# Performance work log

Hardware: AMD Instinct MI355X
Metric: run time of the kernel (lower is better)

Reference implementation:

```python
import jax, jax.numpy as jnp
import numpy as np

N_NODES = 100000
N_EDGES = 1600000
N_GRAPHS = 2048
F_IN = 33
D = 256


def _graph_conv(x, edge_index, w_rel, b_rel, w_root):
    # PyG GraphConv (aggr='add'): out = lin_rel(sum_j x_j) + lin_root(x)
    src, dst = edge_index[0], edge_index[1]
    agg = jax.ops.segment_sum(x[src], dst, num_segments=x.shape[0])  # [N, F]
    return agg @ w_rel + b_rel + x @ w_root


def setup_inputs() -> dict:
    key = jax.random.key(0)
    ks = jax.random.split(key, 16)
    scale_in = 1.0 / np.sqrt(F_IN)
    scale_d = 1.0 / np.sqrt(D)
    inp = {
        "x": jax.random.normal(ks[0], (N_NODES, F_IN), dtype=jnp.float32),
        "edge_index": jax.random.randint(ks[1], (2, N_EDGES), 0, N_NODES),
        "batch_index": jnp.sort(jax.random.randint(ks[2], (N_NODES,), 0, N_GRAPHS)),
        # initial_conv: GraphConv(F_IN -> D)
        "w_rel0": jax.random.normal(ks[3], (F_IN, D), dtype=jnp.float32) * scale_in,
        "b_rel0": jnp.zeros((D,), dtype=jnp.float32),
        "w_root0": jax.random.normal(ks[4], (F_IN, D), dtype=jnp.float32) * scale_in,
        # conv1..conv3: GraphConv(D -> D)
        "w_rel1": jax.random.normal(ks[5], (D, D), dtype=jnp.float32) * scale_d,
        "b_rel1": jnp.zeros((D,), dtype=jnp.float32),
        "w_root1": jax.random.normal(ks[6], (D, D), dtype=jnp.float32) * scale_d,
        "w_rel2": jax.random.normal(ks[7], (D, D), dtype=jnp.float32) * scale_d,
        "b_rel2": jnp.zeros((D,), dtype=jnp.float32),
        "w_root2": jax.random.normal(ks[8], (D, D), dtype=jnp.float32) * scale_d,
        "w_rel3": jax.random.normal(ks[9], (D, D), dtype=jnp.float32) * scale_d,
        "b_rel3": jnp.zeros((D,), dtype=jnp.float32),
        "w_root3": jax.random.normal(ks[10], (D, D), dtype=jnp.float32) * scale_d,
        # output head Linear(D -> 1)
        "w_out": jax.random.normal(ks[11], (D, 1), dtype=jnp.float32) * scale_d,
        "b_out": jnp.zeros((1,), dtype=jnp.float32),
    }
    return inp


def reference(x, edge_index, batch_index,
              w_rel0, b_rel0, w_root0,
              w_rel1, b_rel1, w_root1,
              w_rel2, b_rel2, w_root2,
              w_rel3, b_rel3, w_root3,
              w_out, b_out):
    # dropout omitted (eval mode)
    h = jax.nn.gelu(_graph_conv(x, edge_index, w_rel0, b_rel0, w_root0))
    h = jax.nn.gelu(_graph_conv(h, edge_index, w_rel1, b_rel1, w_root1))
    h = jax.nn.gelu(_graph_conv(h, edge_index, w_rel2, b_rel2, w_root2))
    h = jax.nn.gelu(_graph_conv(h, edge_index, w_rel3, b_rel3, w_root3))
    # global mean pool over graphs
    sums = jax.ops.segment_sum(h, batch_index, num_segments=N_GRAPHS)          # [G, D]
    counts = jax.ops.segment_sum(jnp.ones((h.shape[0],), h.dtype), batch_index,
                                 num_segments=N_GRAPHS)                         # [G]
    pooled = sums / jnp.maximum(counts, 1.0)[:, None]
    return pooled @ w_out + b_out                                               # [G, 1]
```

## Files before the change

kernel.cpp:

```cpp
#include <hip/hip_runtime.h>
#include <math.h>

#define NN 100000
#define NE 1600000
#define NG 2048
#define FIN 33
#define DD 256

#define SH 8
#define NB ((NN + 255) >> 8)
#define CH 4096
#define PCAP 4608
#define ESCAP 6144

#define RBLKS ((NN + 255) / 256)

typedef __attribute__((ext_vector_type(8))) short bf16x8;
typedef __attribute__((ext_vector_type(4))) float f32x4;

__device__ __forceinline__ float b2f(unsigned short u){
    union { unsigned int i; float f; } c; c.i = ((unsigned int)u) << 16; return c.f;
}
__device__ __forceinline__ unsigned short f2b(float f){
    union { float f; unsigned int u; } c; c.f = f;
    unsigned int r = c.u + 0x7fffu + ((c.u >> 16) & 1u);
    return (unsigned short)(r >> 16);
}

__device__ __forceinline__ float gelu_tanh(float x){
    float x3 = x * x * x;
    float t = tanhf(0.7978845608028654f * (x + 0.044715f * x3));
    return 0.5f * x * (1.0f + t);
}

__global__ __launch_bounds__(256) void k_bin(const int* __restrict__ src,
                                             const int* __restrict__ dst,
                                             int* __restrict__ gcur,
                                             int* __restrict__ pairs){
    __shared__ int cnt[NB];
    __shared__ int lb[NB];
    __shared__ int gbase[NB];
    __shared__ int sc[512];
    __shared__ int2 stage[CH];

    int t = threadIdx.x;
    for(int i = t; i < NB; i += 256) cnt[i] = 0;
    __syncthreads();

    int e0 = blockIdx.x * CH;
    int n = NE - e0; if(n > CH) n = CH;

    int  myb[16];
    int  myr[16];
    int2 myp[16];
    #pragma unroll
    for(int k = 0; k < 16; k++){
        int e = e0 + t + k * 256;
        if(e < NE){
            int s = src[e], d = dst[e];
            int b = d >> SH;
            myr[k] = atomicAdd(&cnt[b], 1);
            myb[k] = b;
            myp[k] = make_int2(s, d);
        } else myb[k] = -1;
    }
    __syncthreads();

    sc[t]       = (t       < NB) ? cnt[t]       : 0;
    sc[t + 256] = (t + 256 < NB) ? cnt[t + 256] : 0;
    __syncthreads();
    for(int off = 1; off < 512; off <<= 1){
        int a  = (t >= off)       ? sc[t - off]       : 0;
        int b2 = (t + 256 >= off) ? sc[t + 256 - off] : 0;
        __syncthreads();
        sc[t] += a; sc[t + 256] += b2;
        __syncthreads();
    }
    for(int i = t; i < NB; i += 256){
        lb[i] = sc[i] - cnt[i];
        int c = cnt[i];
        gbase[i] = (c > 0) ? atomicAdd(&gcur[i], c) : 0;
    }
    __syncthreads();

    #pragma unroll
    for(int k = 0; k < 16; k++){
        if(myb[k] >= 0) stage[lb[myb[k]] + myr[k]] = myp[k];
    }
    __syncthreads();

    for(int i = t; i < n; i += 256){
        int2 p = stage[i];
        int b = p.y >> SH;
        int tgt = gbase[b] + (i - lb[b]);
        if(tgt < PCAP) pairs[(size_t)b * PCAP + tgt] = p.x | ((p.y & 255) << 17);
    }
}

__global__ void k_sscan(const int* __restrict__ gcur, int* __restrict__ boff){
    __shared__ int s[512];
    int t = threadIdx.x;
    int v = 0;
    if(t < NB){ v = gcur[t]; if(v > PCAP) v = PCAP; }
    s[t] = v; __syncthreads();
    for(int off = 1; off < 512; off <<= 1){
        int u = (t >= off) ? s[t - off] : 0;
        __syncthreads();
        s[t] += u;
        __syncthreads();
    }
    if(t < NB) boff[t] = s[t] - v;
}

__global__ __launch_bounds__(256) void k_bcsr(const int* __restrict__ pairs,
                                              const int* __restrict__ gcur,
                                              const int* __restrict__ boff,
                                              int* __restrict__ deg,
                                              int* __restrict__ rs,
                                              int* __restrict__ esrc){
    __shared__ int hist[256];
    __shared__ int sc[256];
    __shared__ int cur2[256];
    __shared__ int est[ESCAP];

    int b = blockIdx.x;
    int t = threadIdx.x;
    int m = gcur[b]; if(m > PCAP) m = PCAP;
    int pstart = boff[b];
    const int* bp = pairs + (size_t)b * PCAP;

    hist[t] = 0;
    __syncthreads();
    for(int i = t; i < m; i += 256) atomicAdd(&hist[(bp[i] >> 17) & 255], 1);
    __syncthreads();

    sc[t] = hist[t]; __syncthreads();
    for(int off = 1; off < 256; off <<= 1){
        int u = (t >= off) ? sc[t - off] : 0;
        __syncthreads();
        sc[t] += u;
        __syncthreads();
    }
    int excl = sc[t] - hist[t];
    cur2[t] = excl;
    int node = (b << 8) + t;
    if(node < NN){
        deg[node] = hist[t];
        rs[node]  = pstart + excl;
    }
    __syncthreads();

    for(int i = t; i < m; i += 256){
        int p = bp[i];
        int pos = atomicAdd(&cur2[(p >> 17) & 255], 1);
        int s = p & 0x1FFFF;
        if(pos < ESCAP) est[pos] = s;
        else esrc[pstart + pos] = s;
    }
    __syncthreads();
    int lim = (m < ESCAP) ? m : ESCAP;
    for(int i = t; i < lim; i += 256) esrc[pstart + i] = est[i];
}

__global__ void k_xpad(const float* __restrict__ x, unsigned short* __restrict__ xb){
    int idx = blockIdx.x * 256 + threadIdx.x;
    if(idx >= NN * 64) return;
    int n = idx >> 6, c = idx & 63;
    xb[idx] = (c < FIN) ? f2b(x[(size_t)n * FIN + c]) : 0;
}

__global__ void k_aggx(const unsigned short* __restrict__ xb, const int* __restrict__ rs,
                       const int* __restrict__ deg, const int* __restrict__ esrc,
                       unsigned short* __restrict__ axb){
    int wv = (blockIdx.x * blockDim.x + threadIdx.x) >> 6;
    int lane = threadIdx.x & 63;
    int node = wv * 4 + (lane >> 4);
    int l16 = lane & 15;
    if(node >= NN) return;
    int start = rs[node], cnt = deg[node];
    float a0 = 0.f, a1 = 0.f, a2 = 0.f, a3 = 0.f;
    const unsigned short* xp = xb + l16 * 4;
    int j = 0;
    for(; j + 4 <= cnt; j += 4){
        int e0 = esrc[start+j], e1 = esrc[start+j+1], e2 = esrc[start+j+2], e3 = esrc[start+j+3];
        ushort4 v0 = *(const ushort4*)(xp + (size_t)e0 * 64);
        ushort4 v1 = *(const ushort4*)(xp + (size_t)e1 * 64);
        ushort4 v2 = *(const ushort4*)(xp + (size_t)e2 * 64);
        ushort4 v3 = *(const ushort4*)(xp + (size_t)e3 * 64);
        a0 += (b2f(v0.x) + b2f(v1.x)) + (b2f(v2.x) + b2f(v3.x));
        a1 += (b2f(v0.y) + b2f(v1.y)) + (b2f(v2.y) + b2f(v3.y));
        a2 += (b2f(v0.z) + b2f(v1.z)) + (b2f(v2.z) + b2f(v3.z));
        a3 += (b2f(v0.w) + b2f(v1.w)) + (b2f(v2.w) + b2f(v3.w));
    }
    for(; j < cnt; j++){
        int e = esrc[start + j];
        ushort4 v = *(const ushort4*)(xp + (size_t)e * 64);
        a0 += b2f(v.x); a1 += b2f(v.y); a2 += b2f(v.z); a3 += b2f(v.w);
    }
    ushort4 o; o.x = f2b(a0); o.y = f2b(a1); o.z = f2b(a2); o.w = f2b(a3);
    *(ushort4*)(axb + (size_t)node * 64 + l16 * 4) = o;
}

__global__ void k_agg256(const unsigned short* __restrict__ h, const int* __restrict__ rs,
                         const int* __restrict__ deg, const int* __restrict__ esrc,
                         unsigned short* __restrict__ agg){
    int wv = (blockIdx.x * blockDim.x + threadIdx.x) >> 6;
    int lane = threadIdx.x & 63;
    int node = wv * 2 + (lane >> 5);
    int l32 = lane & 31;
    if(node >= NN) return;
    int start = rs[node], cnt = deg[node];
    float a[8] = {0.f,0.f,0.f,0.f,0.f,0.f,0.f,0.f};
    const unsigned short* hp = h + l32 * 8;
    int j = 0;
    for(; j + 8 <= cnt; j += 8){
        bf16x8 v[8];
        #pragma unroll
        for(int q = 0; q < 8; q++){
            int e = esrc[start + j + q];
            v[q] = *(const bf16x8*)(hp + (size_t)e * DD);
        }
        #pragma unroll
        for(int q = 0; q < 8; q++)
            #pragma unroll
            for(int d = 0; d < 8; d++)
                a[d] += b2f((unsigned short)v[q][d]);
    }
    for(; j < cnt; j++){
        int e = esrc[start + j];
        bf16x8 v = *(const bf16x8*)(hp + (size_t)e * DD);
        #pragma unroll
        for(int d = 0; d < 8; d++) a[d] += b2f((unsigned short)v[d]);
    }
    bf16x8 o;
    #pragma unroll
    for(int d = 0; d < 8; d++) o[d] = (short)f2b(a[d]);
    *(bf16x8*)(agg + (size_t)node * DD + l32 * 8) = o;
}

struct WPtrs { const float* w[6]; };

__global__ void k_wt6(WPtrs wp, unsigned short* __restrict__ btAll){
    __shared__ float s[16][17];
    const float* W = wp.w[blockIdx.z];
    unsigned short* Bt = btAll + (size_t)blockIdx.z * DD * DD;
    int tx = threadIdx.x, ty = threadIdx.y;
    int k = blockIdx.y * 16 + ty;
    int j = blockIdx.x * 16 + tx;
    s[ty][tx] = W[k * DD + j];
    __syncthreads();
    Bt[(size_t)(blockIdx.x * 16 + ty) * DD + blockIdx.y * 16 + tx] = f2b(s[tx][ty]);
}

struct W2Ptrs { const float* w[2]; };

__global__ void k_wt0(W2Ptrs wp, unsigned short* __restrict__ btAll){
    int idx = blockIdx.x * 256 + threadIdx.x;
    if(idx >= DD * 64) return;
    const float* W = wp.w[blockIdx.z];
    unsigned short* Bt = btAll + (size_t)blockIdx.z * DD * 64;
    int j = idx >> 6, k = idx & 63;
    Bt[idx] = (k < FIN) ? f2b(W[(size_t)k * DD + j]) : 0;
}

__global__ void k_cnt(const int* __restrict__ batch, int* __restrict__ gcnt){
    int i = blockIdx.x * 256 + threadIdx.x;
    if(i < NN) atomicAdd(&gcnt[batch[i]], 1);
}

template<int KS, int AST, bool POOL>
__global__ __launch_bounds__(512, 4) void k_mfma_gemm(
    const unsigned short* __restrict__ A0, const unsigned short* __restrict__ A1,
    const unsigned short* __restrict__ Bt0, const unsigned short* __restrict__ Bt1,
    const float* __restrict__ bias, unsigned short* __restrict__ out,
    const int* __restrict__ batch, const float* __restrict__ wout,
    float* __restrict__ gsum)
{
    constexpr int CK  = KS * 32;
    constexpr int BST = CK + 8;
    constexpr int SEG = CK / 8;
    __shared__ unsigned short Bs[128 * BST];

    int t = threadIdx.x;
    int lane = t & 63;
    int w = t >> 6;
    int r16 = lane & 15;
    int kg  = lane >> 4;

    int bid = blockIdx.x;
    int rblk = (bid >> 4) * 8 + (bid & 7);
    int chalf = (bid >> 3) & 1;
    if(rblk >= RBLKS) return;
    int i0 = rblk * 256;
    int jbase = chalf * 128;
    int baseRow = i0 + w * 32;

    f32x4 acc[2][8];
    #pragma unroll
    for(int m = 0; m < 2; m++)
        #pragma unroll
        for(int n = 0; n < 8; n++)
            acc[m][n] = (f32x4){0.f, 0.f, 0.f, 0.f};

    auto loadA = [&](int gks, bf16x8* af){
        const unsigned short* Ap = (gks < KS) ? A0 : A1;
        int kk = ((gks < KS) ? gks : gks - KS) * 32 + kg * 8;
        #pragma unroll
        for(int m = 0; m < 2; m++){
            int gi = baseRow + m * 16 + r16;
            if(gi > NN - 1) gi = NN - 1;
            af[m] = *(const bf16x8*)(Ap + (size_t)gi * AST + kk);
        }
    };

    bf16x8 afb[2][2];
    loadA(0, afb[0]);
    loadA(1, afb[1]);

    #pragma unroll
    for(int c = 0; c < 2; c++){
        const unsigned short* Bp = c ? Bt1 : Bt0;
        if(c) __syncthreads();
        #pragma unroll
        for(int p = 0; p < (128 * SEG) / 512; p++){
            int idx = p * 512 + t;
            int row = idx / SEG;
            int k8 = (idx % SEG) * 8;
            *(bf16x8*)(&Bs[row * BST + k8]) =
                *(const bf16x8*)(Bp + (size_t)(jbase + row) * AST + k8);
        }
        __syncthreads();
        #pragma unroll
        for(int ksl = 0; ksl < KS; ksl++){
            int gks = c * KS + ksl;
            __builtin_amdgcn_s_setprio(1);
            #pragma unroll
            for(int n = 0; n < 8; n++){
                bf16x8 bfr = *(const bf16x8*)(&Bs[(n * 16 + r16) * BST + ksl * 32 + kg * 8]);
                acc[0][n] = __builtin_amdgcn_mfma_f32_16x16x32_bf16(afb[gks & 1][0], bfr, acc[0][n], 0, 0, 0);
                acc[1][n] = __builtin_amdgcn_mfma_f32_16x16x32_bf16(afb[gks & 1][1], bfr, acc[1][n], 0, 0, 0);
            }
            __builtin_amdgcn_s_setprio(0);
            if(gks + 2 < 2 * KS) loadA(gks + 2, afb[gks & 1]);
        }
    }

    int rg = kg * 4;
    if constexpr (!POOL){
        #pragma unroll
        for(int n = 0; n < 8; n++){
            int gj = jbase + n * 16 + r16;
            float bb = bias[gj];
            #pragma unroll
            for(int m = 0; m < 2; m++){
                #pragma unroll
                for(int r = 0; r < 4; r++){
                    int gi = baseRow + m * 16 + rg + r;
                    if(gi < NN)
                        out[(size_t)gi * DD + gj] = f2b(gelu_tanh(acc[m][n][r] + bb));
                }
            }
        }
    } else {
        #pragma unroll
        for(int m = 0; m < 2; m++){
            #pragma unroll
            for(int r = 0; r < 4; r++){
                float s = 0.f;
                #pragma unroll
                for(int n = 0; n < 8; n++){
                    int gj = jbase + n * 16 + r16;
                    s += gelu_tanh(acc[m][n][r] + bias[gj]) * wout[gj];
                }
                s += __shfl_xor(s, 1);
                s += __shfl_xor(s, 2);
                s += __shfl_xor(s, 4);
                s += __shfl_xor(s, 8);
                int gi = baseRow + m * 16 + rg + r;
                if(r16 == 0 && gi < NN)
                    atomicAdd(&gsum[batch[gi]], s);
            }
        }
    }
}

__global__ void k_final(const float* __restrict__ gsum, const int* __restrict__ gcnt,
                        const float* __restrict__ bout, float* __restrict__ out){
    int g = blockIdx.x * 256 + threadIdx.x;
    if(g < NG) out[g] = gsum[g] / fmaxf((float)gcnt[g], 1.f) + bout[0];
}

extern "C" void kernel_launch(void* const* d_in, const int* in_sizes, int n_in,
                              void* d_out, int out_size, void* d_ws, size_t ws_size,
                              hipStream_t stream){
    const float* x       = (const float*)d_in[0];
    const int*   ei      = (const int*)d_in[1];
    const int*   src     = ei;
    const int*   dst     = ei + NE;
    const int*   batch   = (const int*)d_in[2];
    const float* w_rel0  = (const float*)d_in[3];
    const float* b_rel0  = (const float*)d_in[4];
    const float* w_root0 = (const float*)d_in[5];
    const float* w_rel1  = (const float*)d_in[6];
    const float* b_rel1  = (const float*)d_in[7];
    const float* w_root1 = (const float*)d_in[8];
    const float* w_rel2  = (const float*)d_in[9];
    const float* b_rel2  = (const float*)d_in[10];
    const float* w_root2 = (const float*)d_in[11];
    const float* w_rel3  = (const float*)d_in[12];
    const float* b_rel3  = (const float*)d_in[13];
    const float* w_root3 = (const float*)d_in[14];
    const float* w_out   = (const float*)d_in[15];
    const float* b_out   = (const float*)d_in[16];
    float* out = (float*)d_out;

    char* ws = (char*)d_ws;
    size_t off = 0;
    auto alloc = [&](size_t bytes) -> void* {
        void* p = ws + off;
        off = (off + bytes + 255) & ~(size_t)255;
        return p;
    };
    unsigned short* hA  = (unsigned short*)alloc((size_t)NN * DD * 2);
    unsigned short* hB  = (unsigned short*)alloc((size_t)NN * DD * 2);
    unsigned short* agg = (unsigned short*)alloc((size_t)NN * DD * 2);
    int*   deg  = (int*)alloc((size_t)NN * 4);
    int*   rs   = (int*)alloc((size_t)NN * 4);
    int*   esrc = (int*)alloc((size_t)NE * 4);
    int*   gcur = (int*)alloc(512 * 4);
    int*   boff = (int*)alloc(512 * 4);
    float* gsum = (float*)alloc((size_t)NG * 4);
    int*   gcnt = (int*)alloc((size_t)NG * 4);
    unsigned short* btAll = (unsigned short*)alloc((size_t)6 * DD * DD * 2);
    unsigned short* bt0All = (unsigned short*)alloc((size_t)2 * DD * 64 * 2);
    (void)ws_size; (void)in_sizes; (void)n_in; (void)out_size;

    int* pairs = (int*)hB;
    unsigned short* xb  = agg;
    unsigned short* axb = agg + (size_t)NN * 64 + 128;

    hipMemsetAsync(gcur, 0, 512 * 4, stream);
    k_bin<<<(NE + CH - 1) / CH, 256, 0, stream>>>(src, dst, gcur, pairs);
    k_sscan<<<1, 512, 0, stream>>>(gcur, boff);
    k_bcsr<<<NB, 256, 0, stream>>>(pairs, gcur, boff, deg, rs, esrc);

    size_t poolBytes = (size_t)((char*)(gcnt + NG) - (char*)gsum);
    hipMemsetAsync(gsum, 0, poolBytes, stream);
    k_cnt<<<(NN + 255) / 256, 256, 0, stream>>>(batch, gcnt);

    WPtrs wp; wp.w[0] = w_rel1; wp.w[1] = w_root1; wp.w[2] = w_rel2;
    wp.w[3] = w_root2; wp.w[4] = w_rel3; wp.w[5] = w_root3;
    k_wt6<<<dim3(16, 16, 6), dim3(16, 16), 0, stream>>>(wp, btAll);
    W2Ptrs w2; w2.w[0] = w_rel0; w2.w[1] = w_root0;
    k_wt0<<<dim3((DD * 64 + 255) / 256, 1, 2), 256, 0, stream>>>(w2, bt0All);
    k_xpad<<<(NN * 64 + 255) / 256, 256, 0, stream>>>(x, xb);

    unsigned short* bt[6];
    for(int i = 0; i < 6; i++) bt[i] = btAll + (size_t)i * DD * DD;
    unsigned short* bt0r = bt0All;
    unsigned short* bt0o = bt0All + (size_t)DD * 64;

    int agg2Grid = (NN * 32 + 255) / 256;
    int gemmGrid = ((RBLKS + 7) / 8) * 16;

    k_aggx<<<(NN + 15) / 16, 256, 0, stream>>>(xb, rs, deg, esrc, axb);
    k_mfma_gemm<2, 64, false><<<gemmGrid, 512, 0, stream>>>(axb, xb, bt0r, bt0o, b_rel0, hA,
                                                            batch, w_out, gsum);
    k_agg256<<<agg2Grid, 256, 0, stream>>>(hA, rs, deg, esrc, agg);
    k_mfma_gemm<8, 256, false><<<gemmGrid, 512, 0, stream>>>(agg, hA, bt[0], bt[1], b_rel1, hB,
                                                             batch, w_out, gsum);
    k_agg256<<<agg2Grid, 256, 0, stream>>>(hB, rs, deg, esrc, agg);
    k_mfma_gemm<8, 256, false><<<gemmGrid, 512, 0, stream>>>(agg, hB, bt[2], bt[3], b_rel2, hA,
                                                             batch, w_out, gsum);
    k_agg256<<<agg2Grid, 256, 0, stream>>>(hA, rs, deg, esrc, agg);
    k_mfma_gemm<8, 256, true><<<gemmGrid, 512, 0, stream>>>(agg, hA, bt[4], bt[5], b_rel3, hB,
                                                            batch, w_out, gsum);

    k_final<<<(NG + 255) / 256, 256, 0, stream>>>(gsum, gcnt, b_out, out);
}
```

Measured before the change: 776.6 us.

## Fuse neighbor aggregation into GEMM via LDS-staged aggregated tile

Replaces the separate aggregation kernel and GEMM for the 256-wide layers with a fused kernel. Each 128-row block gathers neighbor sums into a swizzled LDS tile, then runs MFMA with B fragments read straight from global memory instead of staged in LDS. This avoids the global round-trip of the aggregated matrix and three kernel launches, at the cost of a 64KB LDS footprint that limits occupancy and B reads that go uncached through LDS. GELU is also rewritten in a sigmoid/exp form, which is algebraically equivalent to the tanh form.

```diff
diff --git a/kernel.cpp b/kernel.cpp
--- a/kernel.cpp
+++ b/kernel.cpp
@@ -14,6 +14,7 @@
 #define ESCAP 6144
 
 #define RBLKS ((NN + 255) / 256)
+#define FBLKS ((NN + 127) / 128)
 
 typedef __attribute__((ext_vector_type(8))) short bf16x8;
 typedef __attribute__((ext_vector_type(4))) float f32x4;
@@ -28,9 +29,8 @@
 }
 
 __device__ __forceinline__ float gelu_tanh(float x){
-    float x3 = x * x * x;
-    float t = tanhf(0.7978845608028654f * (x + 0.044715f * x3));
-    return 0.5f * x * (1.0f + t);
+    float z = 0.7978845608028654f * (x + 0.044715f * x * x * x);
+    return x / (1.0f + __expf(-2.0f * z));
 }
 
 __global__ __launch_bounds__(256) void k_bin(const int* __restrict__ src,
@@ -201,43 +201,6 @@
     *(ushort4*)(axb + (size_t)node * 64 + l16 * 4) = o;
 }
 
-__global__ void k_agg256(const unsigned short* __restrict__ h, const int* __restrict__ rs,
-                         const int* __restrict__ deg, const int* __restrict__ esrc,
-                         unsigned short* __restrict__ agg){
-    int wv = (blockIdx.x * blockDim.x + threadIdx.x) >> 6;
-    int lane = threadIdx.x & 63;
-    int node = wv * 2 + (lane >> 5);
-    int l32 = lane & 31;
-    if(node >= NN) return;
-    int start = rs[node], cnt = deg[node];
-    float a[8] = {0.f,0.f,0.f,0.f,0.f,0.f,0.f,0.f};
-    const unsigned short* hp = h + l32 * 8;
-    int j = 0;
-    for(; j + 8 <= cnt; j += 8){
-        bf16x8 v[8];
-        #pragma unroll
-        for(int q = 0; q < 8; q++){
-            int e = esrc[start + j + q];
-            v[q] = *(const bf16x8*)(hp + (size_t)e * DD);
-        }
-        #pragma unroll
-        for(int q = 0; q < 8; q++)
-            #pragma unroll
-            for(int d = 0; d < 8; d++)
-                a[d] += b2f((unsigned short)v[q][d]);
-    }
-    for(; j < cnt; j++){
-        int e = esrc[start + j];
-        bf16x8 v = *(const bf16x8*)(hp + (size_t)e * DD);
-        #pragma unroll
-        for(int d = 0; d < 8; d++) a[d] += b2f((unsigned short)v[d]);
-    }
-    bf16x8 o;
-    #pragma unroll
-    for(int d = 0; d < 8; d++) o[d] = (short)f2b(a[d]);
-    *(bf16x8*)(agg + (size_t)node * DD + l32 * 8) = o;
-}
-
 struct WPtrs { const float* w[6]; };
 
 __global__ void k_wt6(WPtrs wp, unsigned short* __restrict__ btAll){
@@ -268,15 +231,12 @@
     if(i < NN) atomicAdd(&gcnt[batch[i]], 1);
 }
 
-template<int KS, int AST, bool POOL>
-__global__ __launch_bounds__(512, 4) void k_mfma_gemm(
+__global__ __launch_bounds__(512, 4) void k_gemm0(
     const unsigned short* __restrict__ A0, const unsigned short* __restrict__ A1,
     const unsigned short* __restrict__ Bt0, const unsigned short* __restrict__ Bt1,
-    const float* __restrict__ bias, unsigned short* __restrict__ out,
-    const int* __restrict__ batch, const float* __restrict__ wout,
-    float* __restrict__ gsum)
+    const float* __restrict__ bias, unsigned short* __restrict__ out)
 {
-    constexpr int CK  = KS * 32;
+    constexpr int CK  = 64;
     constexpr int BST = CK + 8;
     constexpr int SEG = CK / 8;
     __shared__ unsigned short Bs[128 * BST];
@@ -303,13 +263,13 @@
             acc[m][n] = (f32x4){0.f, 0.f, 0.f, 0.f};
 
     auto loadA = [&](int gks, bf16x8* af){
-        const unsigned short* Ap = (gks < KS) ? A0 : A1;
-        int kk = ((gks < KS) ? gks : gks - KS) * 32 + kg * 8;
+        const unsigned short* Ap = (gks < 2) ? A0 : A1;
+        int kk = ((gks < 2) ? gks : gks - 2) * 32 + kg * 8;
         #pragma unroll
         for(int m = 0; m < 2; m++){
             int gi = baseRow + m * 16 + r16;
             if(gi > NN - 1) gi = NN - 1;
-            af[m] = *(const bf16x8*)(Ap + (size_t)gi * AST + kk);
+            af[m] = *(const bf16x8*)(Ap + (size_t)gi * 64 + kk);
         }
     };
 
@@ -327,35 +287,150 @@
             int row = idx / SEG;
             int k8 = (idx % SEG) * 8;
             *(bf16x8*)(&Bs[row * BST + k8]) =
-                *(const bf16x8*)(Bp + (size_t)(jbase + row) * AST + k8);
-        }
-        __syncthreads();
-        #pragma unroll
-        for(int ksl = 0; ksl < KS; ksl++){
-            int gks = c * KS + ksl;
-            __builtin_amdgcn_s_setprio(1);
+                *(const bf16x8*)(Bp + (size_t)(jbase + row) * 64 + k8);
+        }
+        __syncthreads();
+        #pragma unroll
+        for(int ksl = 0; ksl < 2; ksl++){
+            int gks = c * 2 + ksl;
             #pragma unroll
             for(int n = 0; n < 8; n++){
                 bf16x8 bfr = *(const bf16x8*)(&Bs[(n * 16 + r16) * BST + ksl * 32 + kg * 8]);
                 acc[0][n] = __builtin_amdgcn_mfma_f32_16x16x32_bf16(afb[gks & 1][0], bfr, acc[0][n], 0, 0, 0);
                 acc[1][n] = __builtin_amdgcn_mfma_f32_16x16x32_bf16(afb[gks & 1][1], bfr, acc[1][n], 0, 0, 0);
             }
-            __builtin_amdgcn_s_setprio(0);
-            if(gks + 2 < 2 * KS) loadA(gks + 2, afb[gks & 1]);
+            if(gks + 2 < 4) loadA(gks + 2, afb[gks & 1]);
+        }
+    }
+
+    int rg = kg * 4;
+    #pragma unroll
+    for(int n = 0; n < 8; n++){
+        int gj = jbase + n * 16 + r16;
+        float bb = bias[gj];
+        #pragma unroll
+        for(int m = 0; m < 2; m++){
+            #pragma unroll
+            for(int r = 0; r < 4; r++){
+                int gi = baseRow + m * 16 + rg + r;
+                if(gi < NN)
+                    out[(size_t)gi * DD + gj] = f2b(gelu_tanh(acc[m][n][r] + bb));
+            }
+        }
+    }
+}
+
+template<bool POOL>
+__global__ __launch_bounds__(512, 4) void k_fused(
+    const unsigned short* __restrict__ h,
+    const int* __restrict__ rs, const int* __restrict__ deg, const int* __restrict__ esrc,
+    const unsigned short* __restrict__ Bt0, const unsigned short* __restrict__ Bt1,
+    const float* __restrict__ bias, unsigned short* __restrict__ out,
+    const int* __restrict__ batch, const float* __restrict__ wout,
+    float* __restrict__ gsum)
+{
+    __shared__ unsigned short As[128 * 256];
+
+    int t = threadIdx.x;
+    int lane = t & 63;
+    int w = t >> 6;
+    int l32 = lane & 31;
+    int r16 = lane & 15;
+    int kg  = lane >> 4;
+    int i0 = blockIdx.x * 128;
+
+    for(int pass = 0; pass < 8; pass++){
+        int rlocal = w * 16 + pass * 2 + (lane >> 5);
+        int node = i0 + rlocal;
+        float a[8] = {0.f,0.f,0.f,0.f,0.f,0.f,0.f,0.f};
+        if(node < NN){
+            int start = rs[node], cnt = deg[node];
+            const unsigned short* hp = h + l32 * 8;
+            int j = 0;
+            for(; j + 8 <= cnt; j += 8){
+                bf16x8 v[8];
+                #pragma unroll
+                for(int q = 0; q < 8; q++){
+                    int e = esrc[start + j + q];
+                    v[q] = *(const bf16x8*)(hp + (size_t)e * DD);
+                }
+                #pragma unroll
+                for(int q = 0; q < 8; q++)
+                    #pragma unroll
+                    for(int d = 0; d < 8; d++)
+                        a[d] += b2f((unsigned short)v[q][d]);
+            }
+            for(; j < cnt; j++){
+                int e = esrc[start + j];
+                bf16x8 v = *(const bf16x8*)(hp + (size_t)e * DD);
+                #pragma unroll
+                for(int d = 0; d < 8; d++) a[d] += b2f((unsigned short)v[d]);
+            }
+        }
+        bf16x8 o;
+        #pragma unroll
+        for(int d = 0; d < 8; d++) o[d] = (short)f2b(a[d]);
+        int byteoff = (rlocal * 256 + l32 * 8) * 2;
+        byteoff ^= (rlocal & 7) << 4;
+        *(bf16x8*)((char*)As + byteoff) = o;
+    }
+    __syncthreads();
+
+    int wr = w >> 2;
+    int wc = w & 3;
+    int jb = wc * 64;
+    int rowBase = wr * 64;
+
+    f32x4 acc[4][4];
+    #pragma unroll
+    for(int m = 0; m < 4; m++)
+        #pragma unroll
+        for(int n = 0; n < 4; n++)
+            acc[m][n] = (f32x4){0.f, 0.f, 0.f, 0.f};
+
+    #pragma unroll
+    for(int c = 0; c < 2; c++){
+        const unsigned short* Bp = c ? Bt1 : Bt0;
+        #pragma unroll
+        for(int ksl = 0; ksl < 8; ksl++){
+            int k8 = ksl * 32 + kg * 8;
+            bf16x8 af[4];
+            if(c == 0){
+                #pragma unroll
+                for(int m = 0; m < 4; m++){
+                    int row = rowBase + m * 16 + r16;
+                    int byteoff = ((row * 256 + k8) * 2) ^ ((row & 7) << 4);
+                    af[m] = *(const bf16x8*)((const char*)As + byteoff);
+                }
+            } else {
+                #pragma unroll
+                for(int m = 0; m < 4; m++){
+                    int gi = i0 + rowBase + m * 16 + r16;
+                    if(gi > NN - 1) gi = NN - 1;
+                    af[m] = *(const bf16x8*)(h + (size_t)gi * DD + k8);
+                }
+            }
+            #pragma unroll
+            for(int n = 0; n < 4; n++){
+                bf16x8 bfr = *(const bf16x8*)(Bp + (size_t)(jb + n * 16 + r16) * DD + k8);
+                #pragma unroll
+                for(int m = 0; m < 4; m++)
+                    acc[m][n] = __builtin_amdgcn_mfma_f32_16x16x32_bf16(af[m], bfr, acc[m][n], 0, 0, 0);
+            }
         }
     }
 
     int rg = kg * 4;
     if constexpr (!POOL){
         #pragma unroll
-        for(int n = 0; n < 8; n++){
-            int gj = jbase + n * 16 + r16;
+        for(int n = 0; n < 4; n++){
+            int gj = jb + n * 16 + r16;
             float bb = bias[gj];
             #pragma unroll
-            for(int m = 0; m < 2; m++){
+            for(int m = 0; m < 4; m++){
                 #pragma unroll
                 for(int r = 0; r < 4; r++){
-                    int gi = baseRow + m * 16 + rg + r;
+                    int gi = i0 + rowBase + m * 16 + rg + r;
                     if(gi < NN)
                         out[(size_t)gi * DD + gj] = f2b(gelu_tanh(acc[m][n][r] + bb));
                 }
@@ -363,20 +438,20 @@
         }
     } else {
         #pragma unroll
-        for(int m = 0; m < 2; m++){
+        for(int m = 0; m < 4; m++){
             #pragma unroll
             for(int r = 0; r < 4; r++){
                 float s = 0.f;
                 #pragma unroll
-                for(int n = 0; n < 8; n++){
-                    int gj = jbase + n * 16 + r16;
+                for(int n = 0; n < 4; n++){
+                    int gj = jb + n * 16 + r16;
                     s += gelu_tanh(acc[m][n][r] + bias[gj]) * wout[gj];
                 }
                 s += __shfl_xor(s, 1);
                 s += __shfl_xor(s, 2);
                 s += __shfl_xor(s, 4);
                 s += __shfl_xor(s, 8);
-                int gi = baseRow + m * 16 + rg + r;
+                int gi = i0 + rowBase + m * 16 + rg + r;
                 if(r16 == 0 && gi < NN)
                     atomicAdd(&gsum[batch[gi]], s);
             }
@@ -460,21 +535,16 @@
     unsigned short* bt0r = bt0All;
     unsigned short* bt0o = bt0All + (size_t)DD * 64;
 
-    int agg2Grid = (NN * 32 + 255) / 256;
-    int gemmGrid = ((RBLKS + 7) / 8) * 16;
+    int gemm0Grid = ((RBLKS + 7) / 8) * 16;
 
     k_aggx<<<(NN + 15) / 16, 256, 0, stream>>>(xb, rs, deg, esrc, axb);
-    k_mfma_gemm<2, 64, false><<<gemmGrid, 512, 0, stream>>>(axb, xb, bt0r, bt0o, b_rel0, hA,
-                                                            batch, w_out, gsum);
-    k_agg256<<<agg2Grid, 256, 0, stream>>>(hA, rs, deg, esrc, agg);
-    k_mfma_gemm<8, 256, false><<<gemmGrid, 512, 0, stream>>>(agg, hA, bt[0], bt[1], b_rel1, hB,
-                                                             batch, w_out, gsum);
-    k_agg256<<<agg2Grid, 256, 0, stream>>>(hB, rs, deg, esrc, agg);
-    k_mfma_gemm<8, 256, false><<<gemmGrid, 512, 0, stream>>>(agg, hB, bt[2], bt[3], b_rel2, hA,
-                                                             batch, w_out, gsum);
-    k_agg256<<<agg2Grid, 256, 0, stream>>>(hA, rs, deg, esrc, agg);
-    k_mfma_gemm<8, 256, true><<<gemmGrid, 512, 0, stream>>>(agg, hA, bt[4], bt[5], b_rel3, hB,
-                                                            batch, w_out, gsum);
+    k_gemm0<<<gemm0Grid, 512, 0, stream>>>(axb, xb, bt0r, bt0o, b_rel0, hA);
+    k_fused<false><<<FBLKS, 512, 0, stream>>>(hA, rs, deg, esrc, bt[0], bt[1], b_rel1, hB,
+                                              batch, w_out, gsum);
+    k_fused<false><<<FBLKS, 512, 0, stream>>>(hB, rs, deg, esrc, bt[2], bt[3], b_rel2, hA,
+                                              batch, w_out, gsum);
+    k_fused<true><<<FBLKS, 512, 0, stream>>>(hA, rs, deg, esrc, bt[4], bt[5], b_rel3, hB,
+                                             batch, w_out, gsum);
 
     k_final<<<(NG + 255) / 256, 256, 0, stream>>>(gsum, gcnt, b_out, out);
 }
```

After: 968.4 us. +24.7%, slower.
